# Kernel tuning notes

Measured on AMD Instinct MI355X. Metric: run time of the kernel, lower is better.

The kernel has to match this reference:

```python
import jax, jax.numpy as jnp
import numpy as np

N = 49152       # nodes
EH = 8192       # hyperedges (star nodes)
M = N + EH
F = 256         # num_features == expan_dim == MLP_hidden
D = 256
HEADS = 8
CHUNK = 1024
NE_N = 10 * N   # nnz of N x N sparse mats
NE_M = 10 * M   # nnz of M x M sparse mats


def spmm(row, col, val, X, n):
    # sparse [n, m] (COO) @ dense X [m, d] -> [n, d]
    return jax.ops.segment_sum(val[:, None] * X[col], row, num_segments=n)


def expan_net(x, row, col, val, Ws, bs, n):
    # 2-layer GCN: (A @ (X @ W) + b), ReLU between; dropout is identity in eval.
    h = spmm(row, col, val, x @ Ws[0], n) + bs[0]
    h = jax.nn.relu(h)
    return spmm(row, col, val, h @ Ws[1], n) + bs[1]


def chunked_mha(q, k, v, in_w, in_b, out_w, out_b):
    # torch nn.MultiheadAttention on unbatched [L, D] chunks of size CHUNK
    n, d = q.shape
    c = n // CHUNK
    dh = d // HEADS
    wq, wk, wv = jnp.split(in_w, 3, axis=0)
    bq, bk, bv = jnp.split(in_b, 3)
    def resh(t):
        return t.reshape(c, CHUNK, HEADS, dh)
    qh = resh(q @ wq.T + bq)
    kh = resh(k @ wk.T + bk)
    vh = resh(v @ wv.T + bv)
    scale = 1.0 / np.sqrt(dh)
    scores = jnp.einsum('clhe,cmhe->chlm', qh, kh) * scale  # [c,H,CHUNK,CHUNK]
    attn = jax.nn.softmax(scores, axis=-1)
    out = jnp.einsum('chlm,cmhe->clhe', attn, vh).reshape(n, d)
    return out @ out_w.T + out_b


def setup_inputs():
    key = jax.random.key(0)
    ks = iter(jax.random.split(key, 64))
    nrm = lambda shape, s=1.0: jax.random.normal(next(ks), shape, dtype=jnp.float32) * s
    uni = lambda shape: jax.random.uniform(next(ks), shape, dtype=jnp.float32)
    ridx = lambda shape, hi: jax.random.randint(next(ks), shape, 0, hi, dtype=jnp.int32)
    inp = {'x': nrm((N, F))}
    for nm, ne, hi in [('A_cg', NE_N, N), ('A_hyp', NE_N, N), ('A_sg', NE_M, M),
                       ('L_cg', NE_N, N), ('L_hyp', NE_N, N), ('L_sg', NE_M, M)]:
        inp[nm + '_row'] = ridx((ne,), hi)
        inp[nm + '_col'] = ridx((ne,), hi)
        inp[nm + '_val'] = uni((ne,)) * 0.1
    for p in ['cg', 'hg', 'sg']:
        inp[p + '_W'] = nrm((2, F, D), 0.05)
        inp[p + '_b'] = nrm((2, D), 0.05)
    for p in ['sn_hyp', 'sn_cg', 'sn_sg']:
        inp[p + '_W'] = nrm((D, D), 0.05)
        inp[p + '_b'] = nrm((D,), 0.05)
    for p in ['spa', 'spe']:
        for q in ['hyp', 'star', 'clq']:
            inp[f'{p}_{q}_W'] = nrm((D, D), 0.05)
            inp[f'{p}_{q}_b'] = nrm((D,), 0.05)
        inp[p + '_in_w'] = nrm((3 * D, D), 0.05)
        inp[p + '_in_b'] = nrm((3 * D,), 0.05)
        inp[p + '_out_w'] = nrm((D, D), 0.05)
        inp[p + '_out_b'] = nrm((D,), 0.05)
    return inp


def reference(x,
              A_cg_row, A_cg_col, A_cg_val, A_hyp_row, A_hyp_col, A_hyp_val,
              A_sg_row, A_sg_col, A_sg_val, L_cg_row, L_cg_col, L_cg_val,
              L_hyp_row, L_hyp_col, L_hyp_val, L_sg_row, L_sg_col, L_sg_val,
              cg_W, cg_b, hg_W, hg_b, sg_W, sg_b,
              sn_hyp_W, sn_hyp_b, sn_cg_W, sn_cg_b, sn_sg_W, sn_sg_b,
              spa_hyp_W, spa_hyp_b, spa_star_W, spa_star_b, spa_clq_W, spa_clq_b,
              spa_in_w, spa_in_b, spa_out_w, spa_out_b,
              spe_hyp_W, spe_hyp_b, spe_star_W, spe_star_b, spe_clq_W, spe_clq_b,
              spe_in_w, spe_in_b, spe_out_w, spe_out_b):
    n = x.shape[0]
    # star features: nodes first, zero-init hyperedge rows (v_mask == [True]*N+[False]*EH)
    x_star = jnp.concatenate([x, jnp.zeros((EH, x.shape[1]), x.dtype)], axis=0)
    # 1. Expansion graph convolutions
    cg_feat = expan_net(x, A_cg_row, A_cg_col, A_cg_val, cg_W, cg_b, n)
    hg_feat = expan_net(x, A_hyp_row, A_hyp_col, A_hyp_val, hg_W, hg_b, n)
    sg_feat = expan_net(x_star, A_sg_row, A_sg_col, A_sg_val, sg_W, sg_b, n + EH)
    X_star, S_star = sg_feat[:n], sg_feat[n:]
    # 2. SmoothNet: linear then Laplacian spmm
    X_hyp = spmm(L_hyp_row, L_hyp_col, L_hyp_val, hg_feat @ sn_hyp_W.T + sn_hyp_b, n)
    X_cg = spmm(L_cg_row, L_cg_col, L_cg_val, cg_feat @ sn_cg_W.T + sn_cg_b, n)
    X_sg = spmm(L_sg_row, L_sg_col, L_sg_val, sg_feat @ sn_sg_W.T + sn_sg_b, n + EH)
    # 3. TAA attention (chunked MHA, Q/K/V = hyp/star/clique projections)
    X_spectral = chunked_mha(X_hyp @ spe_hyp_W.T + spe_hyp_b,
                             X_cg @ spe_star_W.T + spe_star_b,
                             X_sg[:n] @ spe_clq_W.T + spe_clq_b,
                             spe_in_w, spe_in_b, spe_out_w, spe_out_b)
    X_spatial = chunked_mha(hg_feat @ spa_hyp_W.T + spa_hyp_b,
                            cg_feat @ spa_star_W.T + spa_star_b,
                            X_star @ spa_clq_W.T + spa_clq_b,
                            spa_in_w, spa_in_b, spa_out_w, spa_out_b)
    taa = jnp.concatenate([X_spatial, X_spectral], axis=1)
    return taa, X_star, S_star
```

## Files before the change

kernel.cpp:

```cpp
#include <hip/hip_runtime.h>

#define NN 49152
#define EHN 8192
#define MM (NN + EHN)
#define FD 256
#define DD 256
#define NHEADS 8
#define DHEAD 32
#define CHK 1024
#define NEN (10 * NN)
#define NEM (10 * MM)

typedef __bf16 bf16x8 __attribute__((ext_vector_type(8)));
typedef unsigned short u16x8 __attribute__((ext_vector_type(8)));
typedef float f32x4 __attribute__((ext_vector_type(4)));

static __device__ __forceinline__ unsigned short f2bf(float f) {
  unsigned int u = __float_as_uint(f);
  unsigned int r = (u + 0x7FFFu + ((u >> 16) & 1u)) >> 16;
  return (unsigned short)r;
}
static __device__ __forceinline__ float bf2f(unsigned short u) {
  return __uint_as_float((unsigned int)u << 16);
}
static __device__ __forceinline__ unsigned int cvtpk(float a, float b) {
  unsigned int r;
  asm("v_cvt_pk_bf16_f32 %0, %1, %2" : "=v"(r) : "v"(a), "v"(b));
  return r;
}

struct CastJobs {
  const float* src[8];
  unsigned short* dst[8];
  int trans[8];
};
__global__ __launch_bounds__(256) void cast_w8_kernel(CastJobs jobs)
{
  int job = blockIdx.x >> 8;
  int i = (blockIdx.x & 255) * 256 + threadIdx.x;
  int n = i >> 8, k = i & 255;
  const float* src = jobs.src[job];
  float f = jobs.trans[job] ? src[(size_t)k * 256 + n] : src[i];
  jobs.dst[job][i] = f2bf(f);
}

__global__ __launch_bounds__(256) void combine_w_kernel(
    const float* __restrict__ Bw, const float* __restrict__ Aw,
    const float* __restrict__ ab, const float* __restrict__ bb,
    unsigned short* __restrict__ Wc, float* __restrict__ bc, float fscale)
{
  int n = blockIdx.x, t = threadIdx.x;
  __shared__ float shB[256];
  __shared__ float red[256];
  shB[t] = Bw[n * 256 + t];
  __syncthreads();
  float acc = 0.0f;
  #pragma unroll 8
  for (int j = 0; j < 256; ++j) acc += shB[j] * Aw[j * 256 + t];
  Wc[n * 256 + t] = f2bf(acc * fscale);
  red[t] = shB[t] * ab[t];
  __syncthreads();
  for (int off = 128; off; off >>= 1) {
    if (t < off) red[t] += red[t + off];
    __syncthreads();
  }
  if (t == 0) bc[n] = (red[0] + bb[n]) * fscale;
}

__global__ __launch_bounds__(256) void mm256f_kernel(
    const float* __restrict__ A, const float* __restrict__ B,
    float* __restrict__ C)
{
  int n = blockIdx.x, t = threadIdx.x;
  __shared__ float sa[256];
  sa[t] = A[n * 256 + t];
  __syncthreads();
  float acc = 0.0f;
  #pragma unroll 8
  for (int j = 0; j < 256; ++j) acc += sa[j] * B[j * 256 + t];
  C[n * 256 + t] = acc;
}

__global__ __launch_bounds__(256) void mm256b_kernel(
    const float* __restrict__ A, const float* __restrict__ B,
    unsigned short* __restrict__ W, float fs)
{
  int n = blockIdx.x, t = threadIdx.x;
  __shared__ float sa[256];
  sa[t] = A[n * 256 + t];
  __syncthreads();
  float acc = 0.0f;
  #pragma unroll 8
  for (int j = 0; j < 256; ++j) acc += sa[j] * B[j * 256 + t];
  W[n * 256 + t] = f2bf(acc * fs);
}

__global__ __launch_bounds__(256) void mv256_kernel(
    const float* __restrict__ W, const float* __restrict__ v,
    const float* __restrict__ add, float* __restrict__ outv, float fs)
{
  int t = threadIdx.x;
  __shared__ float sv[256];
  sv[t] = v[t];
  __syncthreads();
  float acc = 0.0f;
  #pragma unroll 8
  for (int k = 0; k < 256; ++k) acc += W[t * 256 + k] * sv[k];
  if (add) acc += add[t];
  outv[t] = fs * acc;
}

template<int ABF, int OUTBF>
__global__ __launch_bounds__(256) void gemm2_kernel(
    const void* __restrict__ Ain, const unsigned short* __restrict__ Wt,
    const float* __restrict__ c0, const float* __restrict__ rs,
    const float* __restrict__ cvec, void* __restrict__ Cout,
    int ldc, int coff, int relu)
{
  __shared__ __align__(16) char sA[2][4096];
  __shared__ __align__(16) char sB[2][16384];
  const int tid = threadIdx.x, lane = tid & 63, wid = tid >> 6;
  const int l15 = lane & 15, l4 = lane >> 4;
  const int bm = blockIdx.x * 64;

  f32x4 acc[16] = {};
  const int ar = tid >> 2, akq = (tid & 3) * 8;
  const int bn = tid;

  float4 fa0, fa1;
  u16x8 ua;
  u16x8 rb0, rb1, rb2, rb3;
  auto stage_load = [&](int k0) {
    if (ABF) {
      ua = *(const u16x8*)((const unsigned short*)Ain +
                           (size_t)(bm + ar) * 256 + k0 + akq);
    } else {
      const float* ap = (const float*)Ain + (size_t)(bm + ar) * 256 + k0 + akq;
      fa0 = *(const float4*)ap;
      fa1 = *(const float4*)(ap + 4);
    }
    const unsigned short* bp = Wt + (size_t)bn * 256 + k0;
    rb0 = *(const u16x8*)bp;        rb1 = *(const u16x8*)(bp + 8);
    rb2 = *(const u16x8*)(bp + 16); rb3 = *(const u16x8*)(bp + 24);
  };
  auto stage_write = [&](int buf) {
    u16x8 va;
    if (ABF) {
      va = ua;
    } else {
      va[0] = f2bf(fa0.x); va[1] = f2bf(fa0.y); va[2] = f2bf(fa0.z); va[3] = f2bf(fa0.w);
      va[4] = f2bf(fa1.x); va[5] = f2bf(fa1.y); va[6] = f2bf(fa1.z); va[7] = f2bf(fa1.w);
    }
    int aa = ((ar << 6) + (akq << 1)) ^ ((ar & 7) << 4);
    *(u16x8*)(sA[buf] + aa) = va;
    int bb = (bn << 6) ^ ((bn & 7) << 4);
    *(u16x8*)(sB[buf] + bb) = rb0;
    *(u16x8*)(sB[buf] + (bb ^ 16)) = rb1;
    *(u16x8*)(sB[buf] + (bb ^ 32)) = rb2;
    *(u16x8*)(sB[buf] + (bb ^ 48)) = rb3;
  };

  stage_load(0);
  stage_write(0);
  __syncthreads();
  int cur = 0;
  for (int it = 0; it < 8; ++it) {
    if (it < 7) stage_load((it + 1) * 32);
    int ra = wid * 16 + l15;
    bf16x8 af = *(const bf16x8*)(sA[cur] + ((ra << 6) + (l4 << 4) ^ ((ra & 7) << 4)));
    #pragma unroll
    for (int n4 = 0; n4 < 16; ++n4) {
      int rn = n4 * 16 + l15;
      bf16x8 bf = *(const bf16x8*)(sB[cur] + ((rn << 6) + (l4 << 4) ^ ((rn & 7) << 4)));
      acc[n4] = __builtin_amdgcn_mfma_f32_16x16x32_bf16(af, bf, acc[n4], 0, 0, 0);
    }
    __syncthreads();
    if (it < 7) {
      stage_write(cur ^ 1);
      __syncthreads();
      cur ^= 1;
    }
  }
  const int row = bm + wid * 16 + l4 * 4;
  float rsv[4];
  if (rs) {
    #pragma unroll
    for (int j = 0; j < 4; ++j) rsv[j] = rs[row + j];
  }
  #pragma unroll
  for (int n4 = 0; n4 < 16; ++n4) {
    int col = n4 * 16 + l15;
    float base = c0 ? c0[col] : 0.0f;
    float cv = rs ? cvec[col] : 0.0f;
    #pragma unroll
    for (int j = 0; j < 4; ++j) {
      float v = acc[n4][j] + base;
      if (rs) v += rsv[j] * cv;
      if (relu) v = fmaxf(v, 0.0f);
      if (OUTBF)
        ((unsigned short*)Cout)[(size_t)(row + j) * 256 + col] = f2bf(v);
      else
        ((float*)Cout)[(size_t)(row + j) * ldc + coff + col] = v;
    }
  }
}

__global__ __launch_bounds__(256) void count_kernel(
    const int* __restrict__ rw, int* __restrict__ cnt, int nnz)
{
  int e = blockIdx.x * 256 + threadIdx.x;
  if (e < nnz) atomicAdd(&cnt[rw[e]], 1);
}

__global__ __launch_bounds__(256) void scan1_kernel(
    const int* __restrict__ cnt, int* __restrict__ bsum, int n)
{
  __shared__ int sh[256];
  int i = blockIdx.x * 256 + threadIdx.x;
  sh[threadIdx.x] = (i < n) ? cnt[i] : 0;
  __syncthreads();
  for (int off = 128; off; off >>= 1) {
    if (threadIdx.x < off) sh[threadIdx.x] += sh[threadIdx.x + off];
    __syncthreads();
  }
  if (threadIdx.x == 0) bsum[blockIdx.x] = sh[0];
}

__global__ __launch_bounds__(256) void scan2_kernel(int* __restrict__ bsum, int nb)
{
  __shared__ int sh[256];
  int v = (threadIdx.x < nb) ? bsum[threadIdx.x] : 0;
  sh[threadIdx.x] = v;
  __syncthreads();
  for (int off = 1; off < 256; off <<= 1) {
    int add = (threadIdx.x >= off) ? sh[threadIdx.x - off] : 0;
    __syncthreads();
    sh[threadIdx.x] += add;
    __syncthreads();
  }
  if (threadIdx.x < nb) bsum[threadIdx.x] = sh[threadIdx.x] - v;
}

__global__ __launch_bounds__(256) void scan3_kernel(
    const int* __restrict__ cnt, const int* __restrict__ bsum,
    int* __restrict__ rowptr, int n)
{
  __shared__ int sh[256];
  int i = blockIdx.x * 256 + threadIdx.x;
  int v = (i < n) ? cnt[i] : 0;
  sh[threadIdx.x] = v;
  __syncthreads();
  for (int off = 1; off < 256; off <<= 1) {
    int add = (threadIdx.x >= off) ? sh[threadIdx.x - off] : 0;
    __syncthreads();
    sh[threadIdx.x] += add;
    __syncthreads();
  }
  int incl = sh[threadIdx.x];
  int base = bsum[blockIdx.x];
  if (i < n) rowptr[i] = base + incl - v;
  if (i == n - 1) rowptr[n] = base + incl;
}

__global__ __launch_bounds__(256) void fillcsr_kernel(
    const int* __restrict__ rw, const int* __restrict__ cl,
    const float* __restrict__ vl, const int* __restrict__ rowptr,
    int* __restrict__ cur, int* __restrict__ ecol, float* __restrict__ eval,
    int nnz)
{
  int e = blockIdx.x * 256 + threadIdx.x;
  if (e < nnz) {
    int r = rw[e];
    int pos = rowptr[r] + atomicAdd(&cur[r], 1);
    ecol[pos] = cl[e];
    eval[pos] = vl[e];
  }
}

__global__ __launch_bounds__(256) void rowsum_kernel(
    const int* __restrict__ rowptr, const float* __restrict__ eval,
    float* __restrict__ rs, int n)
{
  int i = blockIdx.x * 256 + threadIdx.x;
  if (i >= n) return;
  float s = 0.0f;
  int end = rowptr[i + 1];
  for (int e = rowptr[i]; e < end; ++e) s += eval[e];
  rs[i] = s;
}

__global__ __launch_bounds__(256) void csr_spmm_kernel(
    const int* __restrict__ rowptr, const int* __restrict__ ecol,
    const float* __restrict__ eval, const unsigned short* __restrict__ X,
    unsigned short* __restrict__ Y, int src_rows,
    const float* __restrict__ bias, int relu, float* __restrict__ Y2)
{
  const int wave = threadIdx.x >> 6, lane = threadIdx.x & 63;
  const int r = blockIdx.x * 4 + wave;
  const int f0 = lane * 4;
  int e = rowptr[r], end = rowptr[r + 1];
  float a0 = 0.0f, a1 = 0.0f, a2 = 0.0f, a3 = 0.0f;
  for (; e + 1 < end; e += 2) {
    int c0i = ecol[e], c1i = ecol[e + 1];
    float v0 = eval[e], v1 = eval[e + 1];
    ushort4 x0 = {0, 0, 0, 0}, x1 = {0, 0, 0, 0};
    if (c0i < src_rows) x0 = *(const ushort4*)(X + (size_t)c0i * DD + f0);
    if (c1i < src_rows) x1 = *(const ushort4*)(X + (size_t)c1i * DD + f0);
    if (c0i < src_rows) {
      a0 += v0 * bf2f(x0.x); a1 += v0 * bf2f(x0.y);
      a2 += v0 * bf2f(x0.z); a3 += v0 * bf2f(x0.w);
    }
    if (c1i < src_rows) {
      a0 += v1 * bf2f(x1.x); a1 += v1 * bf2f(x1.y);
      a2 += v1 * bf2f(x1.z); a3 += v1 * bf2f(x1.w);
    }
  }
  if (e < end) {
    int c = ecol[e];
    float v = eval[e];
    if (c < src_rows) {
      ushort4 xx = *(const ushort4*)(X + (size_t)c * DD + f0);
      a0 += v * bf2f(xx.x); a1 += v * bf2f(xx.y);
      a2 += v * bf2f(xx.z); a3 += v * bf2f(xx.w);
    }
  }
  if (bias) {
    a0 += bias[f0]; a1 += bias[f0 + 1]; a2 += bias[f0 + 2]; a3 += bias[f0 + 3];
  }
  if (relu) {
    a0 = fmaxf(a0, 0.0f); a1 = fmaxf(a1, 0.0f);
    a2 = fmaxf(a2, 0.0f); a3 = fmaxf(a3, 0.0f);
  }
  uint2 yb = { cvtpk(a0, a1), cvtpk(a2, a3) };
  *(uint2*)(Y + (size_t)r * DD + f0) = yb;
  if (Y2) {
    float4 yf = {a0, a1, a2, a3};
    *(float4*)(Y2 + (size_t)r * DD + f0) = yf;
  }
}

__global__ __launch_bounds__(256) void attn_mfma_kernel(
    const unsigned short* __restrict__ Q, const unsigned short* __restrict__ K,
    const unsigned short* __restrict__ V, unsigned short* __restrict__ O)
{
  __shared__ __align__(16) char sKb[4096];
  __shared__ __align__(16) char sVb[4096];
  __shared__ __align__(16) char sPb[8192];
  const int c = blockIdx.z, h = blockIdx.y;
  const int tid = threadIdx.x, lane = tid & 63, wid = tid >> 6;
  const int l15 = lane & 15, l4 = lane >> 4;
  char* sPw = sPb + wid * 2048;
  const size_t base = (size_t)c * (CHK * DD) + (size_t)h * DHEAD;
  const int q0 = blockIdx.x * 64 + wid * 16;

  bf16x8 qf = *(const bf16x8*)(Q + base + (size_t)(q0 + l15) * DD + l4 * 8);

  const int key_s = tid >> 2, dq = (tid & 3) * 8;
  const unsigned short* Kp = K + base + (size_t)key_s * DD + dq;
  const unsigned short* Vp = V + base + (size_t)key_s * DD + dq;
  const int kaddr = ((key_s << 6) + (dq << 1)) ^ ((key_s & 7) << 4);

  f32x4 oacc[2] = {};
  float m = -1e30f, l = 0.0f;
  const f32x4 zero = {};

  for (int kt = 0; kt < CHK; kt += 64) {
    __syncthreads();
    u16x8 kv = *(const u16x8*)Kp;  Kp += 64 * DD;
    u16x8 vv = *(const u16x8*)Vp;  Vp += 64 * DD;
    *(u16x8*)(sKb + kaddr) = kv;
    #pragma unroll
    for (int i = 0; i < 8; ++i) {
      int d = dq + i;
      int bb = ((d << 7) + (key_s << 1))
             ^ ((d & 7) << 4) ^ (((d >> 3) & 3) << 5);
      *(unsigned short*)(sVb + bb) = vv[i];
    }
    __syncthreads();

    f32x4 s[4];
    #pragma unroll
    for (int s4 = 0; s4 < 4; ++s4) {
      int key = s4 * 16 + l15;
      int ba = ((key << 6) + (l4 << 4)) ^ ((key & 7) << 4);
      bf16x8 kf = *(const bf16x8*)(sKb + ba);
      s[s4] = __builtin_amdgcn_mfma_f32_16x16x32_bf16(kf, qf, zero, 0, 0, 0);
    }
    float tmax = -1e30f;
    #pragma unroll
    for (int s4 = 0; s4 < 4; ++s4)
      #pragma unroll
      for (int j = 0; j < 4; ++j) tmax = fmaxf(tmax, s[s4][j]);
    tmax = fmaxf(tmax, __shfl_xor(tmax, 16));
    tmax = fmaxf(tmax, __shfl_xor(tmax, 32));
    float mnew = fmaxf(m, tmax);
    float corr = __builtin_amdgcn_exp2f(m - mnew);
    float psum = 0.0f;
    float p[4][4];
    #pragma unroll
    for (int s4 = 0; s4 < 4; ++s4)
      #pragma unroll
      for (int j = 0; j < 4; ++j) {
        p[s4][j] = __builtin_amdgcn_exp2f(s[s4][j] - mnew);
        psum += p[s4][j];
      }
    psum += __shfl_xor(psum, 16);
    psum += __shfl_xor(psum, 32);
    l = l * corr + psum;
    m = mnew;
    oacc[0] *= corr;
    oacc[1] *= corr;
    #pragma unroll
    for (int s4 = 0; s4 < 4; ++s4) {
      uint2 pk = { cvtpk(p[s4][0], p[s4][1]), cvtpk(p[s4][2], p[s4][3]) };
      int bp = ((l15 << 7) + (s4 << 5) + (l4 << 3)) ^ ((l15 & 7) << 4);
      *(uint2*)(sPw + bp) = pk;
    }
    __syncthreads();

    #pragma unroll
    for (int dh = 0; dh < 2; ++dh)
      #pragma unroll
      for (int kh = 0; kh < 2; ++kh) {
        int d = dh * 16 + l15;
        int ba = ((d << 7) + ((kh * 32 + l4 * 8) << 1))
               ^ ((d & 7) << 4) ^ (((d >> 3) & 3) << 5);
        bf16x8 vf = *(const bf16x8*)(sVb + ba);
        int bp = ((l15 << 7) + (kh << 6) + (l4 << 4)) ^ ((l15 & 7) << 4);
        bf16x8 pf = *(const bf16x8*)(sPw + bp);
        oacc[dh] = __builtin_amdgcn_mfma_f32_16x16x32_bf16(vf, pf, oacc[dh], 0, 0, 0);
      }
  }

  float inv = 1.0f / l;
  unsigned short* orow = O + base + (size_t)(q0 + l15) * DD;
  #pragma unroll
  for (int dh = 0; dh < 2; ++dh) {
    uint2 o2 = { cvtpk(oacc[dh][0] * inv, oacc[dh][1] * inv),
                 cvtpk(oacc[dh][2] * inv, oacc[dh][3] * inv) };
    *(uint2*)(orow + dh * 16 + l4 * 4) = o2;
  }
}

__global__ __launch_bounds__(256) void fill_kernel(float* p, long n, float v)
{
  long i = (long)blockIdx.x * 256 + threadIdx.x;
  if (i < n) p[i] = v;
}

extern "C" void kernel_launch(void* const* d_in, const int* in_sizes, int n_in,
                              void* d_out, int out_size, void* d_ws, size_t ws_size,
                              hipStream_t stream)
{
  const float* x     = (const float*)d_in[0];
  const int*   Acg_r = (const int*)d_in[1];
  const int*   Acg_c = (const int*)d_in[2];
  const float* Acg_v = (const float*)d_in[3];
  const int*   Ahy_r = (const int*)d_in[4];
  const int*   Ahy_c = (const int*)d_in[5];
  const float* Ahy_v = (const float*)d_in[6];
  const int*   Asg_r = (const int*)d_in[7];
  const int*   Asg_c = (const int*)d_in[8];
  const float* Asg_v = (const float*)d_in[9];
  const int*   Lcg_r = (const int*)d_in[10];
  const int*   Lcg_c = (const int*)d_in[11];
  const float* Lcg_v = (const float*)d_in[12];
  const int*   Lhy_r = (const int*)d_in[13];
  const int*   Lhy_c = (const int*)d_in[14];
  const float* Lhy_v = (const float*)d_in[15];
  const int*   Lsg_r = (const int*)d_in[16];
  const int*   Lsg_c = (const int*)d_in[17];
  const float* Lsg_v = (const float*)d_in[18];
  const float* cg_W  = (const float*)d_in[19];
  const float* cg_b  = (const float*)d_in[20];
  const float* hg_W  = (const float*)d_in[21];
  const float* hg_b  = (const float*)d_in[22];
  const float* sg_W  = (const float*)d_in[23];
  const float* sg_b  = (const float*)d_in[24];
  const float* snh_W = (const float*)d_in[25];
  const float* snh_b = (const float*)d_in[26];
  const float* snc_W = (const float*)d_in[27];
  const float* snc_b = (const float*)d_in[28];
  const float* sns_W = (const float*)d_in[29];
  const float* sns_b = (const float*)d_in[30];
  const float* spa_hyp_W  = (const float*)d_in[31];
  const float* spa_hyp_b  = (const float*)d_in[32];
  const float* spa_star_W = (const float*)d_in[33];
  const float* spa_star_b = (const float*)d_in[34];
  const float* spa_clq_W  = (const float*)d_in[35];
  const float* spa_clq_b  = (const float*)d_in[36];
  const float* spa_in_w   = (const float*)d_in[37];
  const float* spa_in_b   = (const float*)d_in[38];
  const float* spa_out_w  = (const float*)d_in[39];
  const float* spa_out_b  = (const float*)d_in[40];
  const float* spe_hyp_W  = (const float*)d_in[41];
  const float* spe_hyp_b  = (const float*)d_in[42];
  const float* spe_star_W = (const float*)d_in[43];
  const float* spe_star_b = (const float*)d_in[44];
  const float* spe_clq_W  = (const float*)d_in[45];
  const float* spe_clq_b  = (const float*)d_in[46];
  const float* spe_in_w   = (const float*)d_in[47];
  const float* spe_in_b   = (const float*)d_in[48];
  const float* spe_out_w  = (const float*)d_in[49];
  const float* spe_out_b  = (const float*)d_in[50];

  float* out = (float*)d_out;

  const size_t NF = (size_t)NN * DD;
  const size_t MF = (size_t)MM * DD;
  const size_t EDG_TOT = 4 * (size_t)NEN + 2 * (size_t)NEM;
  const size_t RP_TOT  = 4 * (size_t)(NN + 1) + 2 * (size_t)(MM + 1);
  const size_t WELEMS  = 14u * 65536u;
  const size_t need = (3 * MF + 9 * NF) * 2
                    + ((size_t)3 * NN + 65536 + 256 + 4096) * 4
                    + (RP_TOT + 2 * EDG_TOT + MM + 256) * 4
                    + WELEMS * 2;

  auto fill = [&](float v) {
    long tot = (long)out_size;
    fill_kernel<<<dim3((unsigned)((tot + 255) / 256)), 256, 0, stream>>>(out, tot, v);
  };
  if (ws_size < need)                        { fill(12.0f); return; }
  if (n_in != 51)                            { fill(16.0f); return; }
  if (in_sizes[0] != NN * FD)                { fill(20.0f); return; }
  if (in_sizes[3] != NEN)                    { fill(24.0f); return; }
  if (in_sizes[9] != NEM)                    { fill(28.0f); return; }
  if (in_sizes[19] != 2 * FD * DD)           { fill(32.0f); return; }
  if (in_sizes[37] != 3 * DD * DD)           { fill(36.0f); return; }
  if (out_size != NN * 512 + NN * DD + EHN * DD) { fill(40.0f); return; }

  unsigned short* T  = (unsigned short*)d_ws;
  unsigned short* H  = T + MF;
  unsigned short* SG = H + MF;
  unsigned short* CG = SG + MF;
  unsigned short* HG = CG + NF;
  unsigned short* LH = HG + NF;
  unsigned short* LC = LH + NF;
  unsigned short* LS = LC + NF;
  unsigned short* QH = LS + NF;
  unsigned short* KH = QH + NF;
  unsigned short* VH = KH + NF;
  unsigned short* AO = VH + NF;

  float* fp = (float*)(AO + NF);
  float* rs_h = fp;            fp += NN;
  float* rs_c = fp;            fp += NN;
  float* rs_s = fp;            fp += NN;
  float* tmp256 = fp;          fp += 65536;
  float* tmpv = fp;            fp += 256;
  float* CB = fp;              fp += 4096;

  int* ip = (int*)fp;
  int* rp_cg  = ip;              ip += NN + 1;
  int* rp_hy  = ip;              ip += NN + 1;
  int* rp_sg  = ip;              ip += MM + 1;
  int* rp_Lcg = ip;              ip += NN + 1;
  int* rp_Lhy = ip;              ip += NN + 1;
  int* rp_Lsg = ip;              ip += MM + 1;
  int* ec_cg  = ip;              ip += NEN;
  int* ec_hy  = ip;              ip += NEN;
  int* ec_sg  = ip;              ip += NEM;
  int* ec_Lcg = ip;              ip += NEN;
  int* ec_Lhy = ip;              ip += NEN;
  int* ec_Lsg = ip;              ip += NEM;
  float* ev_cg  = (float*)ip;    ip += NEN;
  float* ev_hy  = (float*)ip;    ip += NEN;
  float* ev_sg  = (float*)ip;    ip += NEM;
  float* ev_Lcg = (float*)ip;    ip += NEN;
  float* ev_Lhy = (float*)ip;    ip += NEN;
  float* ev_Lsg = (float*)ip;    ip += NEM;
  int* cnt  = ip;                ip += MM;
  int* bsum = ip;                ip += 256;
  unsigned short* WB = (unsigned short*)ip;

  auto wslot = [&](int s) { return WB + (size_t)s * 65536; };
  auto cb    = [&](int s) { return CB + (size_t)s * 256; };

  auto combine = [&](const float* Bw, const float* Aw, const float* ab,
                     const float* bb, unsigned short* Wc, float* bcp, float fs) {
    combine_w_kernel<<<dim3(256), 256, 0, stream>>>(Bw, Aw, ab, bb, Wc, bcp, fs);
  };
  auto combine3 = [&](const float* w3, const float* b3, const float* pW,
                      const float* pb, const float* sW, const float* sb,
                      unsigned short* Wc, float* cvecp, float* c0p, float fs) {
    mm256f_kernel<<<dim3(256), 256, 0, stream>>>(pW, sW, tmp256);
    mm256b_kernel<<<dim3(256), 256, 0, stream>>>(w3, tmp256, Wc, fs);
    mv256_kernel<<<dim3(1), 256, 0, stream>>>(pW, sb, nullptr, tmpv, 1.0f);
    mv256_kernel<<<dim3(1), 256, 0, stream>>>(w3, tmpv, nullptr, cvecp, fs);
    mv256_kernel<<<dim3(1), 256, 0, stream>>>(w3, pb, b3, c0p, fs);
  };
  auto gemm32in = [&](const float* A, const unsigned short* Wt,
                      unsigned short* C, int Mrows) {
    gemm2_kernel<0, 1><<<dim3(Mrows / 64), 256, 0, stream>>>(
        A, Wt, nullptr, nullptr, nullptr, C, 256, 0, 0);
  };
  auto gemmbb = [&](const unsigned short* A, const unsigned short* Wt,
                    const float* c0, unsigned short* C, int Mrows) {
    gemm2_kernel<1, 1><<<dim3(Mrows / 64), 256, 0, stream>>>(
        A, Wt, c0, nullptr, nullptr, C, 256, 0, 0);
  };
  auto gemmrs = [&](const unsigned short* A, const unsigned short* Wt,
                    const float* c0, const float* rs, const float* cvec,
                    unsigned short* C, int Mrows) {
    gemm2_kernel<1, 1><<<dim3(Mrows / 64), 256, 0, stream>>>(
        A, Wt, c0, rs, cvec, C, 256, 0, 0);
  };
  auto gemmout = [&](const unsigned short* A, const unsigned short* Wt,
                     const float* c0, float* C, int coff) {
    gemm2_kernel<1, 0><<<dim3(NN / 64), 256, 0, stream>>>(
        A, Wt, c0, nullptr, nullptr, C, 512, coff, 0);
  };
  auto build_csr = [&](const int* rw, const int* cl, const float* vl, int nnz,
                       int nrows, int* rowptr, int* ecol, float* eval) {
    hipMemsetAsync(cnt, 0, (size_t)nrows * 4, stream);
    count_kernel<<<dim3((nnz + 255) / 256), 256, 0, stream>>>(rw, cnt, nnz);
    int nb = (nrows + 255) / 256;
    scan1_kernel<<<dim3(nb), 256, 0, stream>>>(cnt, bsum, nrows);
    scan2_kernel<<<dim3(1), 256, 0, stream>>>(bsum, nb);
    scan3_kernel<<<dim3(nb), 256, 0, stream>>>(cnt, bsum, rowptr, nrows);
    hipMemsetAsync(cnt, 0, (size_t)nrows * 4, stream);
    fillcsr_kernel<<<dim3((nnz + 255) / 256), 256, 0, stream>>>(
        rw, cl, vl, rowptr, cnt, ecol, eval, nnz);
  };
  auto spmm = [&](const int* rowptr, const int* ecol, const float* eval,
                  const unsigned short* X, unsigned short* Y, int srcR, int dstR,
                  const float* bias, bool relu, float* Y2 = nullptr) {
    csr_spmm_kernel<<<dim3(dstR / 4), 256, 0, stream>>>(
        rowptr, ecol, eval, X, Y, srcR, bias, relu ? 1 : 0, Y2);
  };
  auto attn = [&](const unsigned short* Qp, const unsigned short* Kp,
                  const unsigned short* Vp, unsigned short* Op) {
    attn_mfma_kernel<<<dim3(CHK / 64, NHEADS, NN / CHK), 256, 0, stream>>>(
        Qp, Kp, Vp, Op);
  };

  const float fsQ = 0.17677669529663687f * 1.4426950408889634f;

  {
    CastJobs jobs;
    jobs.src[0] = cg_W;           jobs.dst[0] = wslot(0);  jobs.trans[0] = 1;
    jobs.src[1] = cg_W + FD * DD; jobs.dst[1] = wslot(1);  jobs.trans[1] = 1;
    jobs.src[2] = hg_W;           jobs.dst[2] = wslot(2);  jobs.trans[2] = 1;
    jobs.src[3] = hg_W + FD * DD; jobs.dst[3] = wslot(3);  jobs.trans[3] = 1;
    jobs.src[4] = sg_W;           jobs.dst[4] = wslot(4);  jobs.trans[4] = 1;
    jobs.src[5] = sg_W + FD * DD; jobs.dst[5] = wslot(5);  jobs.trans[5] = 1;
    jobs.src[6] = spa_out_w;      jobs.dst[6] = wslot(12); jobs.trans[6] = 0;
    jobs.src[7] = spe_out_w;      jobs.dst[7] = wslot(13); jobs.trans[7] = 0;
    cast_w8_kernel<<<dim3(8 * 256), 256, 0, stream>>>(jobs);
  }
  combine(spa_in_w,                spa_hyp_W,  spa_hyp_b,  spa_in_b,          wslot(6), cb(0), fsQ);
  combine(spa_in_w + DD * DD,      spa_star_W, spa_star_b, spa_in_b + DD,     wslot(7), cb(1), 1.0f);
  combine(spa_in_w + 2 * DD * DD,  spa_clq_W,  spa_clq_b,  spa_in_b + 2 * DD, wslot(8), cb(2), 1.0f);
  combine3(spe_in_w,               spe_in_b,            spe_hyp_W,  spe_hyp_b,  snh_W, snh_b, wslot(9),  cb(3), cb(4), fsQ);
  combine3(spe_in_w + DD * DD,     spe_in_b + DD,       spe_star_W, spe_star_b, snc_W, snc_b, wslot(10), cb(5), cb(6), 1.0f);
  combine3(spe_in_w + 2 * DD * DD, spe_in_b + 2 * DD,   spe_clq_W,  spe_clq_b,  sns_W, sns_b, wslot(11), cb(7), cb(8), 1.0f);

  build_csr(Acg_r, Acg_c, Acg_v, NEN, NN, rp_cg, ec_cg, ev_cg);
  build_csr(Ahy_r, Ahy_c, Ahy_v, NEN, NN, rp_hy, ec_hy, ev_hy);
  build_csr(Asg_r, Asg_c, Asg_v, NEM, MM, rp_sg, ec_sg, ev_sg);
  build_csr(Lcg_r, Lcg_c, Lcg_v, NEN, NN, rp_Lcg, ec_Lcg, ev_Lcg);
  build_csr(Lhy_r, Lhy_c, Lhy_v, NEN, NN, rp_Lhy, ec_Lhy, ev_Lhy);
  build_csr(Lsg_r, Lsg_c, Lsg_v, NEM, MM, rp_Lsg, ec_Lsg, ev_Lsg);
  rowsum_kernel<<<dim3(NN / 256), 256, 0, stream>>>(rp_Lhy, ev_Lhy, rs_h, NN);
  rowsum_kernel<<<dim3(NN / 256), 256, 0, stream>>>(rp_Lcg, ev_Lcg, rs_c, NN);
  rowsum_kernel<<<dim3(NN / 256), 256, 0, stream>>>(rp_Lsg, ev_Lsg, rs_s, NN);

  gemm32in(x, wslot(0), T, NN);
  spmm(rp_cg, ec_cg, ev_cg, T, H, NN, NN, cg_b, true);
  gemmbb(H, wslot(1), nullptr, T, NN);
  spmm(rp_cg, ec_cg, ev_cg, T, CG, NN, NN, cg_b + DD, false);

  gemm32in(x, wslot(2), T, NN);
  spmm(rp_hy, ec_hy, ev_hy, T, H, NN, NN, hg_b, true);
  gemmbb(H, wslot(3), nullptr, T, NN);
  spmm(rp_hy, ec_hy, ev_hy, T, HG, NN, NN, hg_b + DD, false);

  gemm32in(x, wslot(4), T, NN);
  spmm(rp_sg, ec_sg, ev_sg, T, H, NN, MM, sg_b, true);
  gemmbb(H, wslot(5), nullptr, T, MM);
  spmm(rp_sg, ec_sg, ev_sg, T, SG, MM, MM, sg_b + DD, false, out + (size_t)NN * 512);

  spmm(rp_Lhy, ec_Lhy, ev_Lhy, HG, LH, NN, NN, nullptr, false);
  spmm(rp_Lcg, ec_Lcg, ev_Lcg, CG, LC, NN, NN, nullptr, false);
  spmm(rp_Lsg, ec_Lsg, ev_Lsg, SG, LS, MM, NN, nullptr, false);

  gemmrs(LH, wslot(9),  cb(4), rs_h, cb(3), QH, NN);
  gemmrs(LC, wslot(10), cb(6), rs_c, cb(5), KH, NN);
  gemmrs(LS, wslot(11), cb(8), rs_s, cb(7), VH, NN);
  attn(QH, KH, VH, AO);
  gemmout(AO, wslot(13), spe_out_b, out, 256);

  gemmbb(HG, wslot(6), cb(0), QH, NN);
  gemmbb(CG, wslot(7), cb(1), KH, NN);
  gemmbb(SG, wslot(8), cb(2), VH, NN);
  attn(QH, KH, VH, AO);
  gemmout(AO, wslot(12), spa_out_b, out, 0);
}
```

Baseline: 1.875 ms.

## Batch CSR builds, unroll SpMM gathers, lazy softmax rescale, remap attention blocks

The six COO-to-CSR conversions become one pass over a combined row space: a single memset, one count kernel, one multi-pass scan (scan2 now loops over more than 256 partial sums), one fill kernel and one rowsum kernel, with the counter reset folded into scan3. This removes dozens of small launches and memsets. The CSR SpMM inner loop now issues four gathers per iteration instead of two to expose more memory-level parallelism. The attention kernel gets a flattened 1D grid with a remapped block index for cache locality, and it skips the online-softmax rescale when the running max rises by at most 8 in log2 units. That last change lets unnormalised probabilities grow up to 2^8 before bf16 packing, which may slightly affect precision.

```diff
diff --git a/kernel.cpp b/kernel.cpp
--- a/kernel.cpp
+++ b/kernel.cpp
@@ -10,6 +10,8 @@
 #define CHK 1024
 #define NEN (10 * NN)
 #define NEM (10 * MM)
+#define ROWS_TOT (4 * NN + 2 * MM)
+#define ETOT (4 * NEN + 2 * NEM)
 
 typedef __bf16 bf16x8 __attribute__((ext_vector_type(8)));
 typedef unsigned short u16x8 __attribute__((ext_vector_type(8)));
@@ -205,11 +207,29 @@
   }
 }
 
-__global__ __launch_bounds__(256) void count_kernel(
-    const int* __restrict__ rw, int* __restrict__ cnt, int nnz)
-{
-  int e = blockIdx.x * 256 + threadIdx.x;
-  if (e < nnz) atomicAdd(&cnt[rw[e]], 1);
+struct CooPtrs {
+  const int* rw[6];
+  const int* cl[6];
+  const float* vl[6];
+};
+static __device__ __forceinline__ void coo_block_resolve(
+    int b, int& g, int& eb, int& rb)
+{
+  if      (b < 1920) { g = 0; eb = 0;    rb = 0; }
+  else if (b < 3840) { g = 1; eb = 1920; rb = NN; }
+  else if (b < 6080) { g = 2; eb = 3840; rb = 2 * NN; }
+  else if (b < 8000) { g = 3; eb = 6080; rb = 2 * NN + MM; }
+  else if (b < 9920) { g = 4; eb = 8000; rb = 3 * NN + MM; }
+  else               { g = 5; eb = 9920; rb = 4 * NN + MM; }
+}
+
+__global__ __launch_bounds__(256) void count_all_kernel(
+    CooPtrs coo, int* __restrict__ cnt)
+{
+  int g, eb, rb;
+  coo_block_resolve(blockIdx.x, g, eb, rb);
+  int e = (blockIdx.x - eb) * 256 + threadIdx.x;
+  atomicAdd(&cnt[rb + coo.rw[g][e]], 1);
 }
 
 __global__ __launch_bounds__(256) void scan1_kernel(
@@ -229,21 +249,30 @@
 __global__ __launch_bounds__(256) void scan2_kernel(int* __restrict__ bsum, int nb)
 {
   __shared__ int sh[256];
-  int v = (threadIdx.x < nb) ? bsum[threadIdx.x] : 0;
-  sh[threadIdx.x] = v;
-  __syncthreads();
-  for (int off = 1; off < 256; off <<= 1) {
-    int add = (threadIdx.x >= off) ? sh[threadIdx.x - off] : 0;
-    __syncthreads();
-    sh[threadIdx.x] += add;
-    __syncthreads();
-  }
-  if (threadIdx.x < nb) bsum[threadIdx.x] = sh[threadIdx.x] - v;
+  int t = threadIdx.x;
+  int carry = 0;
+  for (int base = 0; base < nb; base += 256) {
+    int i = base + t;
+    int v = (i < nb) ? bsum[i] : 0;
+    sh[t] = v;
+    __syncthreads();
+    for (int off = 1; off < 256; off <<= 1) {
+      int add = (t >= off) ? sh[t - off] : 0;
+      __syncthreads();
+      sh[t] += add;
+      __syncthreads();
+    }
+    int incl = sh[t];
+    int tot = sh[255];
+    if (i < nb) bsum[i] = carry + incl - v;
+    carry += tot;
+    __syncthreads();
+  }
 }
 
 __global__ __launch_bounds__(256) void scan3_kernel(
     const int* __restrict__ cnt, const int* __restrict__ bsum,
-    int* __restrict__ rowptr, int n)
+    int* __restrict__ rowptr, int* __restrict__ cntz, int n)
 {
   __shared__ int sh[256];
   int i = blockIdx.x * 256 + threadIdx.x;
@@ -258,35 +287,35 @@
   }
   int incl = sh[threadIdx.x];
   int base = bsum[blockIdx.x];
-  if (i < n) rowptr[i] = base + incl - v;
+  if (i < n) { rowptr[i] = base + incl - v; cntz[i] = 0; }
   if (i == n - 1) rowptr[n] = base + incl;
 }
 
-__global__ __launch_bounds__(256) void fillcsr_kernel(
-    const int* __restrict__ rw, const int* __restrict__ cl,
-    const float* __restrict__ vl, const int* __restrict__ rowptr,
-    int* __restrict__ cur, int* __restrict__ ecol, float* __restrict__ eval,
-    int nnz)
-{
-  int e = blockIdx.x * 256 + threadIdx.x;
-  if (e < nnz) {
-    int r = rw[e];
-    int pos = rowptr[r] + atomicAdd(&cur[r], 1);
-    ecol[pos] = cl[e];
-    eval[pos] = vl[e];
-  }
-}
-
-__global__ __launch_bounds__(256) void rowsum_kernel(
-    const int* __restrict__ rowptr, const float* __restrict__ eval,
-    float* __restrict__ rs, int n)
-{
-  int i = blockIdx.x * 256 + threadIdx.x;
-  if (i >= n) return;
+__global__ __launch_bounds__(256) void fill_all_kernel(
+    CooPtrs coo, const int* __restrict__ P, int* __restrict__ cur,
+    int* __restrict__ ecol, float* __restrict__ eval)
+{
+  int g, eb, rb;
+  coo_block_resolve(blockIdx.x, g, eb, rb);
+  int e = (blockIdx.x - eb) * 256 + threadIdx.x;
+  int grow = rb + coo.rw[g][e];
+  int pos = P[grow] + atomicAdd(&cur[grow], 1);
+  ecol[pos] = coo.cl[g][e];
+  eval[pos] = coo.vl[g][e];
+}
+
+__global__ __launch_bounds__(256) void rowsum_all_kernel(
+    const int* __restrict__ P, const float* __restrict__ eval,
+    float* __restrict__ rsAll)
+{
+  int j = blockIdx.x * 256 + threadIdx.x;
+  int g = j / NN;
+  int r = j - g * NN;
+  int grow = (g == 0 ? 2 * NN + MM : g == 1 ? 3 * NN + MM : 4 * NN + MM) + r;
   float s = 0.0f;
-  int end = rowptr[i + 1];
-  for (int e = rowptr[i]; e < end; ++e) s += eval[e];
-  rs[i] = s;
+  int end = P[grow + 1];
+  for (int e = P[grow]; e < end; ++e) s += eval[e];
+  rsAll[j] = s;
 }
 
 __global__ __launch_bounds__(256) void csr_spmm_kernel(
@@ -300,22 +329,20 @@
   const int f0 = lane * 4;
   int e = rowptr[r], end = rowptr[r + 1];
   float a0 = 0.0f, a1 = 0.0f, a2 = 0.0f, a3 = 0.0f;
-  for (; e + 1 < end; e += 2) {
-    int c0i = ecol[e], c1i = ecol[e + 1];
-    float v0 = eval[e], v1 = eval[e + 1];
-    ushort4 x0 = {0, 0, 0, 0}, x1 = {0, 0, 0, 0};
+  for (; e + 3 < end; e += 4) {
+    int c0i = ecol[e], c1i = ecol[e + 1], c2i = ecol[e + 2], c3i = ecol[e + 3];
+    float v0 = eval[e], v1 = eval[e + 1], v2 = eval[e + 2], v3 = eval[e + 3];
+    ushort4 x0 = {0,0,0,0}, x1 = {0,0,0,0}, x2 = {0,0,0,0}, x3 = {0,0,0,0};
     if (c0i < src_rows) x0 = *(const ushort4*)(X + (size_t)c0i * DD + f0);
     if (c1i < src_rows) x1 = *(const ushort4*)(X + (size_t)c1i * DD + f0);
-    if (c0i < src_rows) {
-      a0 += v0 * bf2f(x0.x); a1 += v0 * bf2f(x0.y);
-      a2 += v0 * bf2f(x0.z); a3 += v0 * bf2f(x0.w);
-    }
-    if (c1i < src_rows) {
-      a0 += v1 * bf2f(x1.x); a1 += v1 * bf2f(x1.y);
-      a2 += v1 * bf2f(x1.z); a3 += v1 * bf2f(x1.w);
-    }
-  }
-  if (e < end) {
+    if (c2i < src_rows) x2 = *(const ushort4*)(X + (size_t)c2i * DD + f0);
+    if (c3i < src_rows) x3 = *(const ushort4*)(X + (size_t)c3i * DD + f0);
+    if (c0i < src_rows) { a0 += v0*bf2f(x0.x); a1 += v0*bf2f(x0.y); a2 += v0*bf2f(x0.z); a3 += v0*bf2f(x0.w); }
+    if (c1i < src_rows) { a0 += v1*bf2f(x1.x); a1 += v1*bf2f(x1.y); a2 += v1*bf2f(x1.z); a3 += v1*bf2f(x1.w); }
+    if (c2i < src_rows) { a0 += v2*bf2f(x2.x); a1 += v2*bf2f(x2.y); a2 += v2*bf2f(x2.z); a3 += v2*bf2f(x2.w); }
+    if (c3i < src_rows) { a0 += v3*bf2f(x3.x); a1 += v3*bf2f(x3.y); a2 += v3*bf2f(x3.z); a3 += v3*bf2f(x3.w); }
+  }
+  for (; e < end; ++e) {
     int c = ecol[e];
     float v = eval[e];
     if (c < src_rows) {
@@ -346,12 +373,13 @@
   __shared__ __align__(16) char sKb[4096];
   __shared__ __align__(16) char sVb[4096];
   __shared__ __align__(16) char sPb[8192];
-  const int c = blockIdx.z, h = blockIdx.y;
+  const int wgid = (blockIdx.x & 7) * 768 + (blockIdx.x >> 3);
+  const int qb = wgid & 15, h = (wgid >> 4) & 7, c = wgid >> 7;
   const int tid = threadIdx.x, lane = tid & 63, wid = tid >> 6;
   const int l15 = lane & 15, l4 = lane >> 4;
   char* sPw = sPb + wid * 2048;
   const size_t base = (size_t)c * (CHK * DD) + (size_t)h * DHEAD;
-  const int q0 = blockIdx.x * 64 + wid * 16;
+  const int q0 = qb * 64 + wid * 16;
 
   bf16x8 qf = *(const bf16x8*)(Q + base + (size_t)(q0 + l15) * DD + l4 * 8);
 
@@ -393,8 +421,14 @@
       for (int j = 0; j < 4; ++j) tmax = fmaxf(tmax, s[s4][j]);
     tmax = fmaxf(tmax, __shfl_xor(tmax, 16));
     tmax = fmaxf(tmax, __shfl_xor(tmax, 32));
-    float mnew = fmaxf(m, tmax);
-    float corr = __builtin_amdgcn_exp2f(m - mnew);
+    bool skip = __all(tmax - m <= 8.0f);
+    float mnew = skip ? m : fmaxf(m, tmax);
+    if (!skip) {
+      float corr = __builtin_amdgcn_exp2f(m - mnew);
+      l *= corr;
+      oacc[0] *= corr;
+      oacc[1] *= corr;
+    }
     float psum = 0.0f;
     float p[4][4];
     #pragma unroll
@@ -406,10 +440,8 @@
       }
     psum += __shfl_xor(psum, 16);
     psum += __shfl_xor(psum, 32);
-    l = l * corr + psum;
+    l += psum;
     m = mnew;
-    oacc[0] *= corr;
-    oacc[1] *= corr;
     #pragma unroll
     for (int s4 = 0; s4 < 4; ++s4) {
       uint2 pk = { cvtpk(p[s4][0], p[s4][1]), cvtpk(p[s4][2], p[s4][3]) };
@@ -508,12 +540,10 @@
 
   const size_t NF = (size_t)NN * DD;
   const size_t MF = (size_t)MM * DD;
-  const size_t EDG_TOT = 4 * (size_t)NEN + 2 * (size_t)NEM;
-  const size_t RP_TOT  = 4 * (size_t)(NN + 1) + 2 * (size_t)(MM + 1);
   const size_t WELEMS  = 14u * 65536u;
   const size_t need = (3 * MF + 9 * NF) * 2
                     + ((size_t)3 * NN + 65536 + 256 + 4096) * 4
-                    + (RP_TOT + 2 * EDG_TOT + MM + 256) * 4
+                    + ((size_t)ROWS_TOT + 1 + 2 * (size_t)ETOT + ROWS_TOT + 2048) * 4
                     + WELEMS * 2;
 
   auto fill = [&](float v) {
@@ -543,35 +573,28 @@
   unsigned short* AO = VH + NF;
 
   float* fp = (float*)(AO + NF);
-  float* rs_h = fp;            fp += NN;
-  float* rs_c = fp;            fp += NN;
-  float* rs_s = fp;            fp += NN;
+  float* rsAll = fp;           fp += 3 * NN;
   float* tmp256 = fp;          fp += 65536;
   float* tmpv = fp;            fp += 256;
   float* CB = fp;              fp += 4096;
 
   int* ip = (int*)fp;
-  int* rp_cg  = ip;              ip += NN + 1;
-  int* rp_hy  = ip;              ip += NN + 1;
-  int* rp_sg  = ip;              ip += MM + 1;
-  int* rp_Lcg = ip;              ip += NN + 1;
-  int* rp_Lhy = ip;              ip += NN + 1;
-  int* rp_Lsg = ip;              ip += MM + 1;
-  int* ec_cg  = ip;              ip += NEN;
-  int* ec_hy  = ip;              ip += NEN;
-  int* ec_sg  = ip;              ip += NEM;
-  int* ec_Lcg = ip;              ip += NEN;
-  int* ec_Lhy = ip;              ip += NEN;
-  int* ec_Lsg = ip;              ip += NEM;
-  float* ev_cg  = (float*)ip;    ip += NEN;
-  float* ev_hy  = (float*)ip;    ip += NEN;
-  float* ev_sg  = (float*)ip;    ip += NEM;
-  float* ev_Lcg = (float*)ip;    ip += NEN;
-  float* ev_Lhy = (float*)ip;    ip += NEN;
-  float* ev_Lsg = (float*)ip;    ip += NEM;
-  int* cnt  = ip;                ip += MM;
-  int* bsum = ip;                ip += 256;
+  int* P    = ip;              ip += ROWS_TOT + 1;
+  int* ecol = ip;              ip += ETOT;
+  float* eval = (float*)ip;    ip += ETOT;
+  int* cnt  = ip;              ip += ROWS_TOT;
+  int* bsum = ip;              ip += 2048;
   unsigned short* WB = (unsigned short*)ip;
+
+  int* rp_cg  = P;
+  int* rp_hy  = P + NN;
+  int* rp_sg  = P + 2 * NN;
+  int* rp_Lcg = P + 2 * NN + MM;
+  int* rp_Lhy = P + 3 * NN + MM;
+  int* rp_Lsg = P + 4 * NN + MM;
+  float* rs_c = rsAll;
+  float* rs_h = rsAll + NN;
+  float* rs_s = rsAll + 2 * NN;
 
   auto wslot = [&](int s) { return WB + (size_t)s * 65536; };
   auto cb    = [&](int s) { return CB + (size_t)s * 256; };
@@ -610,28 +633,15 @@
     gemm2_kernel<1, 0><<<dim3(NN / 64), 256, 0, stream>>>(
         A, Wt, c0, nullptr, nullptr, C, 512, coff, 0);
   };
-  auto build_csr = [&](const int* rw, const int* cl, const float* vl, int nnz,
-                       int nrows, int* rowptr, int* ecol, float* eval) {
-    hipMemsetAsync(cnt, 0, (size_t)nrows * 4, stream);
-    count_kernel<<<dim3((nnz + 255) / 256), 256, 0, stream>>>(rw, cnt, nnz);
-    int nb = (nrows + 255) / 256;
-    scan1_kernel<<<dim3(nb), 256, 0, stream>>>(cnt, bsum, nrows);
-    scan2_kernel<<<dim3(1), 256, 0, stream>>>(bsum, nb);
-    scan3_kernel<<<dim3(nb), 256, 0, stream>>>(cnt, bsum, rowptr, nrows);
-    hipMemsetAsync(cnt, 0, (size_t)nrows * 4, stream);
-    fillcsr_kernel<<<dim3((nnz + 255) / 256), 256, 0, stream>>>(
-        rw, cl, vl, rowptr, cnt, ecol, eval, nnz);
-  };
-  auto spmm = [&](const int* rowptr, const int* ecol, const float* eval,
-                  const unsigned short* X, unsigned short* Y, int srcR, int dstR,
-                  const float* bias, bool relu, float* Y2 = nullptr) {
+  auto spmm = [&](const int* rowptr, const unsigned short* X, unsigned short* Y,
+                  int srcR, int dstR, const float* bias, bool relu,
+                  float* Y2 = nullptr) {
     csr_spmm_kernel<<<dim3(dstR / 4), 256, 0, stream>>>(
         rowptr, ecol, eval, X, Y, srcR, bias, relu ? 1 : 0, Y2);
   };
   auto attn = [&](const unsigned short* Qp, const unsigned short* Kp,
                   const unsigned short* Vp, unsigned short* Op) {
-    attn_mfma_kernel<<<dim3(CHK / 64, NHEADS, NN / CHK), 256, 0, stream>>>(
-        Qp, Kp, Vp, Op);
+    attn_mfma_kernel<<<dim3(6144), 256, 0, stream>>>(Qp, Kp, Vp, Op);
   };
 
   const float fsQ = 0.17677669529663687f * 1.4426950408889634f;
@@ -655,34 +665,41 @@
   combine3(spe_in_w + DD * DD,     spe_in_b + DD,       spe_star_W, spe_star_b, snc_W, snc_b, wslot(10), cb(5), cb(6), 1.0f);
   combine3(spe_in_w + 2 * DD * DD, spe_in_b + 2 * DD,   spe_clq_W,  spe_clq_b,  sns_W, sns_b, wslot(11), cb(7), cb(8), 1.0f);
 
-  build_csr(Acg_r, Acg_c, Acg_v, NEN, NN, rp_cg, ec_cg, ev_cg);
-  build_csr(Ahy_r, Ahy_c, Ahy_v, NEN, NN, rp_hy, ec_hy, ev_hy);
-  build_csr(Asg_r, Asg_c, Asg_v, NEM, MM, rp_sg, ec_sg, ev_sg);
-  build_csr(Lcg_r, Lcg_c, Lcg_v, NEN, NN, rp_Lcg, ec_Lcg, ev_Lcg);
-  build_csr(Lhy_r, Lhy_c, Lhy_v, NEN, NN, rp_Lhy, ec_Lhy, ev_Lhy);
-  build_csr(Lsg_r, Lsg_c, Lsg_v, NEM, MM, rp_Lsg, ec_Lsg, ev_Lsg);
-  rowsum_kernel<<<dim3(NN / 256), 256, 0, stream>>>(rp_Lhy, ev_Lhy, rs_h, NN);
-  rowsum_kernel<<<dim3(NN / 256), 256, 0, stream>>>(rp_Lcg, ev_Lcg, rs_c, NN);
-  rowsum_kernel<<<dim3(NN / 256), 256, 0, stream>>>(rp_Lsg, ev_Lsg, rs_s, NN);
+  {
+    CooPtrs coo;
+    coo.rw[0] = Acg_r; coo.cl[0] = Acg_c; coo.vl[0] = Acg_v;
+    coo.rw[1] = Ahy_r; coo.cl[1] = Ahy_c; coo.vl[1] = Ahy_v;
+    coo.rw[2] = Asg_r; coo.cl[2] = Asg_c; coo.vl[2] = Asg_v;
+    coo.rw[3] = Lcg_r; coo.cl[3] = Lcg_c; coo.vl[3] = Lcg_v;
+    coo.rw[4] = Lhy_r; coo.cl[4] = Lhy_c; coo.vl[4] = Lhy_v;
+    coo.rw[5] = Lsg_r; coo.cl[5] = Lsg_c; coo.vl[5] = Lsg_v;
+    hipMemsetAsync(cnt, 0, (size_t)ROWS_TOT * 4, stream);
+    count_all_kernel<<<dim3(ETOT / 256), 256, 0, stream>>>(coo, cnt);
+    scan1_kernel<<<dim3(ROWS_TOT / 256), 256, 0, stream>>>(cnt, bsum, ROWS_TOT);
+    scan2_kernel<<<dim3(1), 256, 0, stream>>>(bsum, ROWS_TOT / 256);
+    scan3_kernel<<<dim3(ROWS_TOT / 256), 256, 0, stream>>>(cnt, bsum, P, cnt, ROWS_TOT);
+    fill_all_kernel<<<dim3(ETOT / 256), 256, 0, stream>>>(coo, P, cnt, ecol, eval);
+    rowsum_all_kernel<<<dim3(3 * NN / 256), 256, 0, stream>>>(P, eval, rsAll);
+  }
 
   gemm32in(x, wslot(0), T, NN);
-  spmm(rp_cg, ec_cg, ev_cg, T, H, NN, NN, cg_b, true);
+  spmm(rp_cg, T, H, NN, NN, cg_b, true);
   gemmbb(H, wslot(1), nullptr, T, NN);
-  spmm(rp_cg, ec_cg, ev_cg, T, CG, NN, NN, cg_b + DD, false);
+  spmm(rp_cg, T, CG, NN, NN, cg_b + DD, false);
 
   gemm32in(x, wslot(2), T, NN);
-  spmm(rp_hy, ec_hy, ev_hy, T, H, NN, NN, hg_b, true);
+  spmm(rp_hy, T, H, NN, NN, hg_b, true);
   gemmbb(H, wslot(3), nullptr, T, NN);
-  spmm(rp_hy, ec_hy, ev_hy, T, HG, NN, NN, hg_b + DD, false);
+  spmm(rp_hy, T, HG, NN, NN, hg_b + DD, false);
 
   gemm32in(x, wslot(4), T, NN);
-  spmm(rp_sg, ec_sg, ev_sg, T, H, NN, MM, sg_b, true);
+  spmm(rp_sg, T, H, NN, MM, sg_b, true);
   gemmbb(H, wslot(5), nullptr, T, MM);
-  spmm(rp_sg, ec_sg, ev_sg, T, SG, MM, MM, sg_b + DD, false, out + (size_t)NN * 512);
-
-  spmm(rp_Lhy, ec_Lhy, ev_Lhy, HG, LH, NN, NN, nullptr, false);
-  spmm(rp_Lcg, ec_Lcg, ev_Lcg, CG, LC, NN, NN, nullptr, false);
-  spmm(rp_Lsg, ec_Lsg, ev_Lsg, SG, LS, MM, NN, nullptr, false);
+  spmm(rp_sg, T, SG, MM, MM, sg_b + DD, false, out + (size_t)NN * 512);
+
+  spmm(rp_Lhy, HG, LH, NN, NN, nullptr, false);
+  spmm(rp_Lcg, CG, LC, NN, NN, nullptr, false);
+  spmm(rp_Lsg, SG, LS, MM, NN, nullptr, false);
 
   gemmrs(LH, wslot(9),  cb(4), rs_h, cb(3), QH, NN);
   gemmrs(LC, wslot(10), cb(6), rs_c, cb(5), KH, NN);
```

Measured after the change: 1.677 ms. -10.6%, faster.
